# Performance work log

Measured on AMD Instinct MI355X. Metric: run time of the kernel, lower is better.

## Reference

```python
import jax, jax.numpy as jnp
import numpy as np

N_NODES = 50000
N_EDGES = 800000
IN_DIM = 128
OUT_DIM = 64
NEG_SLOPE = 0.01  # torch F.leaky_relu default


def setup_inputs() -> dict:
    key = jax.random.key(0)
    k1, k2, k3, k4, k5 = jax.random.split(key, 5)
    features = jax.random.normal(k1, (N_NODES, IN_DIM), dtype=jnp.float32)
    # xavier-ish scale for weights
    fc_w = jax.random.normal(k2, (OUT_DIM, IN_DIM), dtype=jnp.float32) * (1.0 / np.sqrt(IN_DIM))
    attn_w = jax.random.normal(k3, (2 * OUT_DIM,), dtype=jnp.float32) * (1.0 / np.sqrt(2 * OUT_DIM))
    src = jax.random.randint(k4, (N_EDGES,), 0, N_NODES, dtype=jnp.int32)
    dst = jax.random.randint(k5, (N_EDGES,), 0, N_NODES, dtype=jnp.int32)
    return {"features": features, "fc_w": fc_w, "attn_w": attn_w, "src": src, "dst": dst}


def reference(features, fc_w, attn_w, src, dst):
    n = features.shape[0]
    out_dim = fc_w.shape[0]
    # z = fc(features), [N, out_dim]
    z = features @ fc_w.T
    # attn_fc([z_src || z_dst]) = z_src @ w_src + z_dst @ w_dst
    a_src = z @ attn_w[:out_dim]   # [N]
    a_dst = z @ attn_w[out_dim:]   # [N]
    e = a_src[src] + a_dst[dst]    # [E] per-edge raw score
    e = jnp.where(e > 0, e, NEG_SLOPE * e)  # leaky_relu
    # edge softmax over incoming edges of each dst node
    e_max = jax.ops.segment_max(e, dst, num_segments=n)      # [N]
    w = jnp.exp(e - e_max[dst])                               # [E]
    denom = jax.ops.segment_sum(w, dst, num_segments=n)       # [N]
    # weighted neighbor sum: sum_e alpha_e * z[src_e]
    num = jax.ops.segment_sum(w[:, None] * z[src], dst, num_segments=n)  # [N, out_dim]
    h = num / jnp.where(denom > 0, denom, 1.0)[:, None]
    # activation = elu
    h = jax.nn.elu(h)
    return h
```

## Files before the change

kernel.cpp:

```cpp
#include <hip/hip_runtime.h>
#include <hip/hip_bf16.h>
#include <hip/hip_fp16.h>

#define N_NODES 50000
#define N_EDGES 800000
#define IN_DIM 128
#define OUT_DIM 64
#define NEG_SLOPE 0.01f
#define NEG_INF (-3.0e38f)

#define N_STRIPS (N_NODES / 16)
#define Z_BLOCKS ((N_STRIPS + 3) / 4)
#define E_I4 (N_EDGES / 4)

#define NB ((N_NODES + 127) / 128)
#define CAP_B 3072
#define CNT_STRIDE 16
#define EB 100
#define CHUNK_I4 (E_I4 / EB)

typedef __bf16 bf16x8 __attribute__((ext_vector_type(8)));
typedef float f32x4 __attribute__((ext_vector_type(4)));

__device__ __forceinline__ unsigned short f2bf_us(float f) {
  __hip_bfloat16 h = __float2bfloat16(f);
  return *reinterpret_cast<unsigned short*>(&h);
}
__device__ __forceinline__ bf16x8 pack_bf16(float4 lo, float4 hi) {
  union { bf16x8 v; unsigned short u[8]; } r;
  r.u[0] = f2bf_us(lo.x); r.u[1] = f2bf_us(lo.y);
  r.u[2] = f2bf_us(lo.z); r.u[3] = f2bf_us(lo.w);
  r.u[4] = f2bf_us(hi.x); r.u[5] = f2bf_us(hi.y);
  r.u[6] = f2bf_us(hi.z); r.u[7] = f2bf_us(hi.w);
  return r.v;
}
__device__ __forceinline__ float bflo(unsigned u) {
  return __uint_as_float(u << 16);
}
__device__ __forceinline__ float bfhi(unsigned u) {
  return __uint_as_float(u & 0xffff0000u);
}

__global__ __launch_bounds__(256) void gat_z_bucket(
    const float* __restrict__ feat, const float* __restrict__ fcw,
    const float* __restrict__ attnw, __hip_bfloat16* __restrict__ z,
    float* __restrict__ asrc, float* __restrict__ adst,
    const int* __restrict__ src, const int* __restrict__ dst,
    int* __restrict__ cnt, unsigned* __restrict__ pairs) {
  if (blockIdx.x >= Z_BLOCKS) {
    __shared__ int hist[NB];
    __shared__ int curs[NB];
    const int tid = threadIdx.x;
    const int i0 = (blockIdx.x - Z_BLOCKS) * CHUNK_I4;
    for (int i = tid; i < NB; i += 256) hist[i] = 0;
    __syncthreads();
    for (int t = i0 + tid; t < i0 + CHUNK_I4; t += 256) {
      int4 d = ((const int4*)dst)[t];
      atomicAdd(&hist[d.x >> 7], 1);
      atomicAdd(&hist[d.y >> 7], 1);
      atomicAdd(&hist[d.z >> 7], 1);
      atomicAdd(&hist[d.w >> 7], 1);
    }
    __syncthreads();
    for (int i = tid; i < NB; i += 256) {
      int h = hist[i];
      curs[i] = h ? atomicAdd(cnt + i * CNT_STRIDE, h) : 0;
    }
    __syncthreads();
    for (int t = i0 + tid; t < i0 + CHUNK_I4; t += 256) {
      int4 s = ((const int4*)src)[t];
      int4 d = ((const int4*)dst)[t];
#define BKT_PUT(dd, ss)                                                    \
  {                                                                        \
    int b = (dd) >> 7;                                                     \
    int r = atomicAdd(&curs[b], 1);                                        \
    if (r < CAP_B)                                                         \
      pairs[(size_t)b * CAP_B + r] =                                       \
          ((unsigned)((dd) & 127) << 16) | (unsigned)(ss);                 \
  }
      BKT_PUT(d.x, s.x)
      BKT_PUT(d.y, s.y)
      BKT_PUT(d.z, s.z)
      BKT_PUT(d.w, s.w)
#undef BKT_PUT
    }
    return;
  }

  const int lane = threadIdx.x & 63;
  const int m = lane & 15;
  const int quad = lane >> 4;
  const int wv = blockIdx.x * 4 + (threadIdx.x >> 6);
  if (wv >= N_STRIPS) return;
  const int n0 = wv * 16;

  bf16x8 bfrag[4][4];
#pragma unroll
  for (int t = 0; t < 4; ++t) {
    const float* wr = fcw + (size_t)(m + 16 * t) * IN_DIM + quad * 8;
#pragma unroll
    for (int c = 0; c < 4; ++c) {
      float4 lo = *(const float4*)(wr + c * 32);
      float4 hi = *(const float4*)(wr + c * 32 + 4);
      bfrag[t][c] = pack_bf16(lo, hi);
    }
  }

  f32x4 acc[4] = {{0.f, 0.f, 0.f, 0.f}, {0.f, 0.f, 0.f, 0.f},
                  {0.f, 0.f, 0.f, 0.f}, {0.f, 0.f, 0.f, 0.f}};
  const float* ar = feat + (size_t)(n0 + m) * IN_DIM + quad * 8;
#pragma unroll
  for (int c = 0; c < 4; ++c) {
    float4 lo = *(const float4*)(ar + c * 32);
    float4 hi = *(const float4*)(ar + c * 32 + 4);
    const bf16x8 af = pack_bf16(lo, hi);
#pragma unroll
    for (int t = 0; t < 4; ++t)
      acc[t] = __builtin_amdgcn_mfma_f32_16x16x32_bf16(af, bfrag[t][c],
                                                       acc[t], 0, 0, 0);
  }

#pragma unroll
  for (int t = 0; t < 4; ++t)
#pragma unroll
    for (int r = 0; r < 4; ++r)
      z[(size_t)(n0 + quad * 4 + r) * OUT_DIM + m + 16 * t] =
          __float2bfloat16(acc[t][r]);

  float aws[4], awd[4];
#pragma unroll
  for (int t = 0; t < 4; ++t) {
    aws[t] = attnw[m + 16 * t];
    awd[t] = attnw[OUT_DIM + m + 16 * t];
  }
  float ps[4], pd[4];
#pragma unroll
  for (int r = 0; r < 4; ++r) {
    float s = 0.f, d = 0.f;
#pragma unroll
    for (int t = 0; t < 4; ++t) {
      s = fmaf(acc[t][r], aws[t], s);
      d = fmaf(acc[t][r], awd[t], d);
    }
    ps[r] = s;
    pd[r] = d;
  }
#pragma unroll
  for (int off = 1; off < 16; off <<= 1) {
#pragma unroll
    for (int r = 0; r < 4; ++r) {
      ps[r] += __shfl_xor(ps[r], off, 64);
      pd[r] += __shfl_xor(pd[r], off, 64);
    }
  }
  if (m == 0) {
#pragma unroll
    for (int r = 0; r < 4; ++r) {
      asrc[n0 + quad * 4 + r] = ps[r];
      adst[n0 + quad * 4 + r] = pd[r];
    }
  }
}

__global__ __launch_bounds__(512) void gat_csr_agg(
    const unsigned* __restrict__ pairs, const int* __restrict__ cnt,
    const __hip_bfloat16* __restrict__ zb, const float* __restrict__ asrc,
    const float* __restrict__ adst, float* __restrict__ out) {
  __shared__ int hist[64];
  __shared__ int noff[65];
  __shared__ int cur[64];
  __shared__ int lsrc[CAP_B];
  const int tid = threadIdx.x;
  const int b = blockIdx.x >> 1;
  const int half = blockIdx.x & 1;
  const int c = min(cnt[b * CNT_STRIDE], CAP_B);
  const unsigned* __restrict__ bp = pairs + (size_t)b * CAP_B;

  if (tid < 64) hist[tid] = 0;
  __syncthreads();
  for (int i = tid; i < c; i += 512) {
    const int ln = (int)(bp[i] >> 16);
    if ((ln >> 6) == half) atomicAdd(&hist[ln & 63], 1);
  }
  __syncthreads();
  if (tid < 64) {
    const int h = hist[tid];
    int s = h;
#pragma unroll
    for (int off = 1; off < 64; off <<= 1) {
      const int u = __shfl_up(s, off, 64);
      if (tid >= off) s += u;
    }
    noff[tid] = s - h;
    cur[tid] = s - h;
    if (tid == 63) noff[64] = s;
  }
  __syncthreads();
  for (int i = tid; i < c; i += 512) {
    const unsigned p = bp[i];
    const int ln = (int)(p >> 16);
    if ((ln >> 6) == half) {
      const int r = atomicAdd(&cur[ln & 63], 1);
      lsrc[r] = (int)(p & 0xFFFFu);
    }
  }
  __syncthreads();

  const int lane = tid & 63;
  const int wv = tid >> 6;
  const int j = lane & 7;
  const int eg = lane >> 3;
  const uint4* __restrict__ zp4 = (const uint4*)zb;

#pragma unroll 1
  for (int k = 0; k < 8; ++k) {
    const int ln = wv * 8 + k;
    const int node = b * 128 + half * 64 + ln;
    if (node >= N_NODES) break;
    const int o0 = noff[ln];
    const int o1 = noff[ln + 1];
    float4* __restrict__ orow = (float4*)(out + (size_t)node * OUT_DIM);
    if (o0 == o1) {
      if (eg == 0) {
        const float4 zv = {0.f, 0.f, 0.f, 0.f};
        orow[2 * j] = zv;
        orow[2 * j + 1] = zv;
      }
      continue;
    }
    const float ad = adst[node];

    float m = NEG_INF, dsum = 0.f;
    float acca[8] = {0.f, 0.f, 0.f, 0.f, 0.f, 0.f, 0.f, 0.f};
    float accb[8] = {0.f, 0.f, 0.f, 0.f, 0.f, 0.f, 0.f, 0.f};

    for (int base = o0; base < o1; base += 64) {
      const int cnt2 = min(64, o1 - base);
      int s = 0;
      float ev = NEG_INF;
      if (lane < cnt2) {
        s = lsrc[base + lane];
        const float v = asrc[s] + ad;
        ev = v > 0.f ? v : NEG_SLOPE * v;
      }
      float cm = ev;
#pragma unroll
      for (int off = 32; off; off >>= 1)
        cm = fmaxf(cm, __shfl_xor(cm, off, 64));
      const float nm = fmaxf(m, cm);
      const float scale = __expf(m - nm);
      dsum *= scale;
#pragma unroll
      for (int cc = 0; cc < 8; ++cc) {
        acca[cc] *= scale;
        accb[cc] *= scale;
      }
      m = nm;

      const float w = (lane < cnt2) ? __expf(ev - m) : 0.f;
      dsum += w;
      const unsigned pk =
          (unsigned)s |
          ((unsigned)__half_as_ushort(__float2half(w)) << 16);

      const int ngr = (cnt2 + 7) >> 3;
      for (int g = 0; g < ngr; g += 2) {
        const unsigned pa = __shfl(pk, 8 * g + eg, 64);
        const int sa = (int)(pa & 0xFFFFu);
        const float wa =
            __half2float(__ushort_as_half((unsigned short)(pa >> 16)));
        const uint4 ua = zp4[(size_t)sa * 8 + j];
        if (g + 1 < ngr) {
          const unsigned pb = __shfl(pk, 8 * (g + 1) + eg, 64);
          const int sb = (int)(pb & 0xFFFFu);
          const float wb =
              __half2float(__ushort_as_half((unsigned short)(pb >> 16)));
          const uint4 ub = zp4[(size_t)sb * 8 + j];
          accb[0] = fmaf(wb, bflo(ub.x), accb[0]);
          accb[1] = fmaf(wb, bfhi(ub.x), accb[1]);
          accb[2] = fmaf(wb, bflo(ub.y), accb[2]);
          accb[3] = fmaf(wb, bfhi(ub.y), accb[3]);
          accb[4] = fmaf(wb, bflo(ub.z), accb[4]);
          accb[5] = fmaf(wb, bfhi(ub.z), accb[5]);
          accb[6] = fmaf(wb, bflo(ub.w), accb[6]);
          accb[7] = fmaf(wb, bfhi(ub.w), accb[7]);
        }
        acca[0] = fmaf(wa, bflo(ua.x), acca[0]);
        acca[1] = fmaf(wa, bfhi(ua.x), acca[1]);
        acca[2] = fmaf(wa, bflo(ua.y), acca[2]);
        acca[3] = fmaf(wa, bfhi(ua.y), acca[3]);
        acca[4] = fmaf(wa, bflo(ua.z), acca[4]);
        acca[5] = fmaf(wa, bfhi(ua.z), acca[5]);
        acca[6] = fmaf(wa, bflo(ua.w), acca[6]);
        acca[7] = fmaf(wa, bfhi(ua.w), acca[7]);
      }
    }

    float acc[8];
#pragma unroll
    for (int cc = 0; cc < 8; ++cc) acc[cc] = acca[cc] + accb[cc];
#pragma unroll
    for (int off = 8; off < 64; off <<= 1)
#pragma unroll
      for (int cc = 0; cc < 8; ++cc) acc[cc] += __shfl_xor(acc[cc], off, 64);
#pragma unroll
    for (int off = 32; off; off >>= 1) dsum += __shfl_xor(dsum, off, 64);

    if (eg == 0) {
      const float inv = 1.f / (dsum > 0.f ? dsum : 1.f);
      float4 r0, r1;
      float h;
      h = acc[0] * inv; r0.x = h > 0.f ? h : expm1f(h);
      h = acc[1] * inv; r0.y = h > 0.f ? h : expm1f(h);
      h = acc[2] * inv; r0.z = h > 0.f ? h : expm1f(h);
      h = acc[3] * inv; r0.w = h > 0.f ? h : expm1f(h);
      h = acc[4] * inv; r1.x = h > 0.f ? h : expm1f(h);
      h = acc[5] * inv; r1.y = h > 0.f ? h : expm1f(h);
      h = acc[6] * inv; r1.z = h > 0.f ? h : expm1f(h);
      h = acc[7] * inv; r1.w = h > 0.f ? h : expm1f(h);
      orow[2 * j] = r0;
      orow[2 * j + 1] = r1;
    }
  }
}

extern "C" void kernel_launch(void* const* d_in, const int* in_sizes, int n_in,
                              void* d_out, int out_size, void* d_ws, size_t ws_size,
                              hipStream_t stream) {
  const float* feat  = (const float*)d_in[0];
  const float* fcw   = (const float*)d_in[1];
  const float* attnw = (const float*)d_in[2];
  const int* src     = (const int*)d_in[3];
  const int* dst     = (const int*)d_in[4];
  float* out = (float*)d_out;

  char* ws = (char*)d_ws;
  __hip_bfloat16* z = (__hip_bfloat16*)ws;
  ws += (size_t)N_NODES * OUT_DIM * sizeof(__hip_bfloat16);
  float* asrc = (float*)ws;   ws += (size_t)N_NODES * sizeof(float);
  float* adst = (float*)ws;   ws += (size_t)N_NODES * sizeof(float);
  int* cnt = (int*)ws;        ws += (size_t)NB * CNT_STRIDE * sizeof(int);
  unsigned* pairs = (unsigned*)ws; ws += (size_t)NB * CAP_B * sizeof(unsigned);

  hipMemsetAsync(cnt, 0, (size_t)NB * CNT_STRIDE * sizeof(int), stream);

  gat_z_bucket<<<Z_BLOCKS + EB, 256, 0, stream>>>(
      feat, fcw, attnw, z, asrc, adst, src, dst, cnt, pairs);
  gat_csr_agg<<<NB * 2, 512, 0, stream>>>(pairs, cnt, z, asrc, adst, out);
}
```

Measured before the change: 149.3 us.

## Map one 16-lane group per destination node and split buckets four ways

The aggregation kernel now assigns each destination node to a 16-lane sub-group, so a wave handles four nodes at once instead of looping over eight nodes with a full wave each. Each bucket is split across four blocks of 32 nodes rather than two blocks of 64, and each lane accumulates 16 output features from two 16-byte loads per edge. The edge-bucketing grid (EB) is also doubled. The goal is to stop wasting lanes on low-degree nodes, where about 16 edges per node left most of a 64-lane wave idle. The cost is that every block rescans its whole bucket to build its local CSR, so that scan is now repeated four times per bucket.

```diff
diff --git a/kernel.cpp b/kernel.cpp
--- a/kernel.cpp
+++ b/kernel.cpp
@@ -16,7 +16,7 @@
 #define NB ((N_NODES + 127) / 128)
 #define CAP_B 3072
 #define CNT_STRIDE 16
-#define EB 100
+#define EB 200
 #define CHUNK_I4 (E_I4 / EB)
 
 typedef __bf16 bf16x8 __attribute__((ext_vector_type(8)));
@@ -166,41 +166,41 @@
     const unsigned* __restrict__ pairs, const int* __restrict__ cnt,
     const __hip_bfloat16* __restrict__ zb, const float* __restrict__ asrc,
     const float* __restrict__ adst, float* __restrict__ out) {
-  __shared__ int hist[64];
-  __shared__ int noff[65];
-  __shared__ int cur[64];
+  __shared__ int hist[32];
+  __shared__ int noff[33];
+  __shared__ int cur[32];
   __shared__ int lsrc[CAP_B];
   const int tid = threadIdx.x;
-  const int b = blockIdx.x >> 1;
-  const int half = blockIdx.x & 1;
+  const int b = blockIdx.x >> 2;
+  const int q = blockIdx.x & 3;
   const int c = min(cnt[b * CNT_STRIDE], CAP_B);
   const unsigned* __restrict__ bp = pairs + (size_t)b * CAP_B;
 
-  if (tid < 64) hist[tid] = 0;
+  if (tid < 32) hist[tid] = 0;
   __syncthreads();
   for (int i = tid; i < c; i += 512) {
     const int ln = (int)(bp[i] >> 16);
-    if ((ln >> 6) == half) atomicAdd(&hist[ln & 63], 1);
+    if ((ln >> 5) == q) atomicAdd(&hist[ln & 31], 1);
   }
   __syncthreads();
-  if (tid < 64) {
+  if (tid < 32) {
     const int h = hist[tid];
     int s = h;
 #pragma unroll
-    for (int off = 1; off < 64; off <<= 1) {
+    for (int off = 1; off < 32; off <<= 1) {
       const int u = __shfl_up(s, off, 64);
       if (tid >= off) s += u;
     }
     noff[tid] = s - h;
     cur[tid] = s - h;
-    if (tid == 63) noff[64] = s;
+    if (tid == 31) noff[32] = s;
   }
   __syncthreads();
   for (int i = tid; i < c; i += 512) {
     const unsigned p = bp[i];
     const int ln = (int)(p >> 16);
-    if ((ln >> 6) == half) {
-      const int r = atomicAdd(&cur[ln & 63], 1);
+    if ((ln >> 5) == q) {
+      const int r = atomicAdd(&cur[ln & 31], 1);
       lsrc[r] = (int)(p & 0xFFFFu);
     }
   }
@@ -208,118 +208,106 @@
 
   const int lane = tid & 63;
   const int wv = tid >> 6;
-  const int j = lane & 7;
-  const int eg = lane >> 3;
+  const int g = lane >> 4;
+  const int sl = lane & 15;
+  const int j2 = sl & 3;
+  const int eg = sl >> 2;
+  const int gbase = lane & 48;
+
+  const int ln = wv * 4 + g;
+  const int node = b * 128 + q * 32 + ln;
+  if (node >= N_NODES) return;
+
   const uint4* __restrict__ zp4 = (const uint4*)zb;
-
-#pragma unroll 1
-  for (int k = 0; k < 8; ++k) {
-    const int ln = wv * 8 + k;
-    const int node = b * 128 + half * 64 + ln;
-    if (node >= N_NODES) break;
-    const int o0 = noff[ln];
-    const int o1 = noff[ln + 1];
-    float4* __restrict__ orow = (float4*)(out + (size_t)node * OUT_DIM);
-    if (o0 == o1) {
-      if (eg == 0) {
-        const float4 zv = {0.f, 0.f, 0.f, 0.f};
-        orow[2 * j] = zv;
-        orow[2 * j + 1] = zv;
-      }
-      continue;
-    }
-    const float ad = adst[node];
-
-    float m = NEG_INF, dsum = 0.f;
-    float acca[8] = {0.f, 0.f, 0.f, 0.f, 0.f, 0.f, 0.f, 0.f};
-    float accb[8] = {0.f, 0.f, 0.f, 0.f, 0.f, 0.f, 0.f, 0.f};
-
-    for (int base = o0; base < o1; base += 64) {
-      const int cnt2 = min(64, o1 - base);
-      int s = 0;
-      float ev = NEG_INF;
-      if (lane < cnt2) {
-        s = lsrc[base + lane];
-        const float v = asrc[s] + ad;
-        ev = v > 0.f ? v : NEG_SLOPE * v;
-      }
-      float cm = ev;
-#pragma unroll
-      for (int off = 32; off; off >>= 1)
-        cm = fmaxf(cm, __shfl_xor(cm, off, 64));
-      const float nm = fmaxf(m, cm);
-      const float scale = __expf(m - nm);
-      dsum *= scale;
-#pragma unroll
-      for (int cc = 0; cc < 8; ++cc) {
-        acca[cc] *= scale;
-        accb[cc] *= scale;
-      }
-      m = nm;
-
-      const float w = (lane < cnt2) ? __expf(ev - m) : 0.f;
-      dsum += w;
-      const unsigned pk =
-          (unsigned)s |
-          ((unsigned)__half_as_ushort(__float2half(w)) << 16);
-
-      const int ngr = (cnt2 + 7) >> 3;
-      for (int g = 0; g < ngr; g += 2) {
-        const unsigned pa = __shfl(pk, 8 * g + eg, 64);
-        const int sa = (int)(pa & 0xFFFFu);
-        const float wa =
-            __half2float(__ushort_as_half((unsigned short)(pa >> 16)));
-        const uint4 ua = zp4[(size_t)sa * 8 + j];
-        if (g + 1 < ngr) {
-          const unsigned pb = __shfl(pk, 8 * (g + 1) + eg, 64);
-          const int sb = (int)(pb & 0xFFFFu);
-          const float wb =
-              __half2float(__ushort_as_half((unsigned short)(pb >> 16)));
-          const uint4 ub = zp4[(size_t)sb * 8 + j];
-          accb[0] = fmaf(wb, bflo(ub.x), accb[0]);
-          accb[1] = fmaf(wb, bfhi(ub.x), accb[1]);
-          accb[2] = fmaf(wb, bflo(ub.y), accb[2]);
-          accb[3] = fmaf(wb, bfhi(ub.y), accb[3]);
-          accb[4] = fmaf(wb, bflo(ub.z), accb[4]);
-          accb[5] = fmaf(wb, bfhi(ub.z), accb[5]);
-          accb[6] = fmaf(wb, bflo(ub.w), accb[6]);
-          accb[7] = fmaf(wb, bfhi(ub.w), accb[7]);
-        }
-        acca[0] = fmaf(wa, bflo(ua.x), acca[0]);
-        acca[1] = fmaf(wa, bfhi(ua.x), acca[1]);
-        acca[2] = fmaf(wa, bflo(ua.y), acca[2]);
-        acca[3] = fmaf(wa, bfhi(ua.y), acca[3]);
-        acca[4] = fmaf(wa, bflo(ua.z), acca[4]);
-        acca[5] = fmaf(wa, bfhi(ua.z), acca[5]);
-        acca[6] = fmaf(wa, bflo(ua.w), acca[6]);
-        acca[7] = fmaf(wa, bfhi(ua.w), acca[7]);
-      }
-    }
-
-    float acc[8];
-#pragma unroll
-    for (int cc = 0; cc < 8; ++cc) acc[cc] = acca[cc] + accb[cc];
-#pragma unroll
-    for (int off = 8; off < 64; off <<= 1)
-#pragma unroll
-      for (int cc = 0; cc < 8; ++cc) acc[cc] += __shfl_xor(acc[cc], off, 64);
-#pragma unroll
-    for (int off = 32; off; off >>= 1) dsum += __shfl_xor(dsum, off, 64);
-
-    if (eg == 0) {
-      const float inv = 1.f / (dsum > 0.f ? dsum : 1.f);
-      float4 r0, r1;
+  const int o0 = noff[ln];
+  const int o1 = noff[ln + 1];
+  float4* __restrict__ orow = (float4*)(out + (size_t)node * OUT_DIM);
+  if (o0 == o1) {
+    if (sl < 4) {
+      const float4 zv = {0.f, 0.f, 0.f, 0.f};
+#pragma unroll
+      for (int v = 0; v < 4; ++v) orow[4 * sl + v] = zv;
+    }
+    return;
+  }
+  const float ad = adst[node];
+
+  float m = NEG_INF, dsum = 0.f;
+  float acc[16];
+#pragma unroll
+  for (int cc = 0; cc < 16; ++cc) acc[cc] = 0.f;
+
+  for (int base = o0; base < o1; base += 16) {
+    const int cnt2 = min(16, o1 - base);
+    int s = 0;
+    float ev = NEG_INF;
+    if (sl < cnt2) {
+      s = lsrc[base + sl];
+      const float v = asrc[s] + ad;
+      ev = v > 0.f ? v : NEG_SLOPE * v;
+    }
+    float cm = ev;
+#pragma unroll
+    for (int off = 1; off < 16; off <<= 1)
+      cm = fmaxf(cm, __shfl_xor(cm, off, 64));
+    const float nm = fmaxf(m, cm);
+    const float scale = __expf(m - nm);
+    dsum *= scale;
+#pragma unroll
+    for (int cc = 0; cc < 16; ++cc) acc[cc] *= scale;
+    m = nm;
+
+    const float w = (sl < cnt2) ? __expf(ev - m) : 0.f;
+    dsum += w;
+    const unsigned pk =
+        (unsigned)s |
+        ((unsigned)__half_as_ushort(__float2half(w)) << 16);
+
+    const int ngr = (cnt2 + 3) >> 2;
+    for (int gg = 0; gg < ngr; ++gg) {
+      const unsigned pa = __shfl(pk, gbase + 4 * gg + eg, 64);
+      const int sa = (int)(pa & 0xFFFFu);
+      const float wa =
+          __half2float(__ushort_as_half((unsigned short)(pa >> 16)));
+      const uint4 ua = zp4[(size_t)sa * 8 + 2 * j2];
+      const uint4 ub = zp4[(size_t)sa * 8 + 2 * j2 + 1];
+      acc[0] = fmaf(wa, bflo(ua.x), acc[0]);
+      acc[1] = fmaf(wa, bfhi(ua.x), acc[1]);
+      acc[2] = fmaf(wa, bflo(ua.y), acc[2]);
+      acc[3] = fmaf(wa, bfhi(ua.y), acc[3]);
+      acc[4] = fmaf(wa, bflo(ua.z), acc[4]);
+      acc[5] = fmaf(wa, bfhi(ua.z), acc[5]);
+      acc[6] = fmaf(wa, bflo(ua.w), acc[6]);
+      acc[7] = fmaf(wa, bfhi(ua.w), acc[7]);
+      acc[8] = fmaf(wa, bflo(ub.x), acc[8]);
+      acc[9] = fmaf(wa, bfhi(ub.x), acc[9]);
+      acc[10] = fmaf(wa, bflo(ub.y), acc[10]);
+      acc[11] = fmaf(wa, bfhi(ub.y), acc[11]);
+      acc[12] = fmaf(wa, bflo(ub.z), acc[12]);
+      acc[13] = fmaf(wa, bfhi(ub.z), acc[13]);
+      acc[14] = fmaf(wa, bflo(ub.w), acc[14]);
+      acc[15] = fmaf(wa, bfhi(ub.w), acc[15]);
+    }
+  }
+
+#pragma unroll
+  for (int off = 4; off <= 8; off <<= 1)
+#pragma unroll
+    for (int cc = 0; cc < 16; ++cc) acc[cc] += __shfl_xor(acc[cc], off, 64);
+#pragma unroll
+  for (int off = 1; off < 16; off <<= 1) dsum += __shfl_xor(dsum, off, 64);
+
+  if (eg == 0) {
+    const float inv = 1.f / (dsum > 0.f ? dsum : 1.f);
+#pragma unroll
+    for (int v = 0; v < 4; ++v) {
+      float4 r;
       float h;
-      h = acc[0] * inv; r0.x = h > 0.f ? h : expm1f(h);
-      h = acc[1] * inv; r0.y = h > 0.f ? h : expm1f(h);
-      h = acc[2] * inv; r0.z = h > 0.f ? h : expm1f(h);
-      h = acc[3] * inv; r0.w = h > 0.f ? h : expm1f(h);
-      h = acc[4] * inv; r1.x = h > 0.f ? h : expm1f(h);
-      h = acc[5] * inv; r1.y = h > 0.f ? h : expm1f(h);
-      h = acc[6] * inv; r1.z = h > 0.f ? h : expm1f(h);
-      h = acc[7] * inv; r1.w = h > 0.f ? h : expm1f(h);
-      orow[2 * j] = r0;
-      orow[2 * j + 1] = r1;
+      h = acc[4 * v + 0] * inv; r.x = h > 0.f ? h : expm1f(h);
+      h = acc[4 * v + 1] * inv; r.y = h > 0.f ? h : expm1f(h);
+      h = acc[4 * v + 2] * inv; r.z = h > 0.f ? h : expm1f(h);
+      h = acc[4 * v + 3] * inv; r.w = h > 0.f ? h : expm1f(h);
+      orow[4 * j2 + v] = r;
     }
   }
 }
@@ -346,5 +334,5 @@
 
   gat_z_bucket<<<Z_BLOCKS + EB, 256, 0, stream>>>(
       feat, fcw, attnw, z, asrc, adst, src, dst, cnt, pairs);
-  gat_csr_agg<<<NB * 2, 512, 0, stream>>>(pairs, cnt, z, asrc, adst, out);
-}
+  gat_csr_agg<<<NB * 4, 512, 0, stream>>>(pairs, cnt, z, asrc, adst, out);
+}
```

Measured after the change: 133.8 us. 1.12x faster.
